# Kernel tuning notes

Measured on AMD Instinct MI355X. Metric: run time of the kernel, lower is better.

Reference implementation:

```python
import math
import jax, jax.numpy as jnp
import numpy as np

NUM_HEADS = 32
HEAD_DIM = 128
POOL = 16
MAX_REL = 8192
RMS_EPS = 1e-6


def _central_mask_features(distances, feature_size, seq_length):
    # center_widths = arange(F) + geomspace(1, seq_length-F+1, F, endpoint=False)
    log_end = math.log(float(seq_length - feature_size + 1))
    log_step = log_end / feature_size
    exponents = jnp.arange(feature_size, dtype=jnp.float32) * log_step
    center_widths = jnp.arange(feature_size, dtype=jnp.float32) + jnp.exp(exponents)
    return (center_widths > distances[..., None]).astype(jnp.float32)


def _shift(x, query_length, key_length):
    # x: [..., n_rows, n_diags] with n_diags = 2*n_rows
    batch_shape = x.shape[:-2]
    n_rows, n_diags = x.shape[-2], x.shape[-1]
    x = x.reshape(*batch_shape, n_diags, n_rows)
    x = x[..., 1:, :]
    x = x.reshape(*batch_shape, n_rows, n_diags - 1)
    return x[..., :key_length]


def setup_inputs() -> dict:
    key = jax.random.key(0)
    ks = jax.random.split(key, 12)
    B, S, D = 1, 8192, 1536
    HD = NUM_HEADS * HEAD_DIM  # 4096
    s = 0.02
    return {
        "x": jax.random.normal(ks[0], (B, S, D), jnp.float32),
        "w_rms": jnp.ones((D,), jnp.float32),
        "W_q": jax.random.normal(ks[1], (D, HD), jnp.float32) * s,
        "W_k": jax.random.normal(ks[2], (D, HD), jnp.float32) * s,
        "W_pos": jax.random.normal(ks[3], (2 * NUM_HEADS, HD), jnp.float32) * s,
        "b_pos": jnp.zeros((HD,), jnp.float32),
        "q_r_bias": jax.random.normal(ks[4], (1, 1, NUM_HEADS, HEAD_DIM), jnp.float32) * s,
        "k_r_bias": jax.random.normal(ks[5], (1, 1, NUM_HEADS, HEAD_DIM), jnp.float32) * s,
        "W_yq": jax.random.normal(ks[6], (D, HEAD_DIM), jnp.float32) * s,
        "W_yk": jax.random.normal(ks[7], (D, HEAD_DIM), jnp.float32) * s,
        "W_pair": jax.random.normal(ks[8], (NUM_HEADS, HEAD_DIM), jnp.float32) * s,
        "b_pair": jnp.zeros((HEAD_DIM,), jnp.float32),
    }


def reference(x, w_rms, W_q, W_k, W_pos, b_pos, q_r_bias, k_r_bias, W_yq, W_yk, W_pair, b_pair):
    B, S, D = x.shape
    Sp = S // POOL
    # mean-pool along sequence (kernel=stride=16)
    x_pooled = x.reshape(B, Sp, POOL, D).mean(axis=2)
    # RMSNorm
    x_norm = x_pooled * jax.lax.rsqrt(jnp.mean(x_pooled * x_pooled, axis=-1, keepdims=True) + RMS_EPS) * w_rms

    q = (x_norm @ W_q).reshape(B, Sp, NUM_HEADS, HEAD_DIM)
    k = (x_norm @ W_k).reshape(B, Sp, NUM_HEADS, HEAD_DIM)

    # relative-position features
    range_vec = jnp.arange(-Sp, Sp, dtype=jnp.float32)
    pos_feat = _central_mask_features(jnp.abs(range_vec), NUM_HEADS, MAX_REL // POOL)  # [2Sp, H]
    sign = jnp.sign(range_vec)[:, None]
    pos_feat = jnp.concatenate([pos_feat, sign * pos_feat], axis=-1)  # [2Sp, 2H]
    pos_enc = (pos_feat @ W_pos + b_pos).reshape(2 * Sp, NUM_HEADS, HEAD_DIM)

    term_q = jnp.einsum('bqhc,phc->bhqp', q + q_r_bias, pos_enc)
    term_k = jnp.einsum('bkhc,phc->bhkp', k + k_r_bias, pos_enc)
    rel_q_a = _shift(term_q, Sp, Sp)  # [B,H,Q,K]
    rel_k_a = _shift(term_k, Sp, Sp)
    rel_q_a = jnp.transpose(rel_q_a, (0, 2, 3, 1))  # [B,Q,K,H]
    rel_k_a = jnp.transpose(rel_k_a, (0, 3, 2, 1))  # [B,P,K,H]

    a = jnp.einsum('bqhc,bkhc->bqkh', q, k)
    a = a + 0.5 * (rel_q_a + rel_k_a)

    x_gelu = jax.nn.gelu(x_norm, approximate=False)
    y_q = x_gelu @ W_yq  # [B,Sp,HEAD_DIM]
    y_k = x_gelu @ W_yk

    pair_act = a @ W_pair + b_pair + y_q[:, :, None, :] + y_k[:, None, :, :]
    return pair_act
```

## Files before the change

### kernel.cpp

```cpp
#include <hip/hip_runtime.h>
#include <hip/hip_bf16.h>
#include <math.h>
#include <stdint.h>

#define NHEADS 32
#define HDIM 128
#define POOLW 16
#define DMODEL 1536
#define SPOOL 512
#define HDTOT 4096
#define PEROWS 1024
#define NPAIR (SPOOL * SPOOL)
#define TCOLS 80

typedef __hip_bfloat16 bf16;
typedef short short8 __attribute__((ext_vector_type(8)));
typedef float f32x4 __attribute__((ext_vector_type(4)));

__device__ __forceinline__ float b2f(const bf16 v) { return __bfloat162float(v); }
__device__ __forceinline__ bf16 f2b(float v) { return __float2bfloat16(v); }
__device__ __forceinline__ short f2bs(float v) {
  bf16 b = __float2bfloat16(v);
  return *reinterpret_cast<short*>(&b);
}

__device__ __forceinline__ void gload_lds16(const void* g, void* l) {
  const __attribute__((address_space(1))) uint32_t* gp =
      (const __attribute__((address_space(1))) uint32_t*)(uintptr_t)g;
  __attribute__((address_space(3))) uint32_t* lp =
      (__attribute__((address_space(3))) uint32_t*)(uintptr_t)l;
  __builtin_amdgcn_global_load_lds(gp, lp, 16, 0, 0);
}

__global__ __launch_bounds__(256) void pool_suffix(
    const float* __restrict__ x, const float* __restrict__ w_rms,
    const float* __restrict__ W_pos,
    bf16* __restrict__ xn, bf16* __restrict__ xg,
    float* __restrict__ SW0, float* __restrict__ SW1) {
  if (blockIdx.x >= SPOOL) {
    int j = (blockIdx.x - SPOOL) * 256 + threadIdx.x;
    float s0 = 0.f, s1 = 0.f;
    SW0[32 * HDTOT + j] = 0.f;
    SW1[32 * HDTOT + j] = 0.f;
    for (int f = 31; f >= 0; --f) {
      s0 += W_pos[f * HDTOT + j];
      s1 += W_pos[(NHEADS + f) * HDTOT + j];
      SW0[f * HDTOT + j] = s0;
      SW1[f * HDTOT + j] = s1;
    }
    return;
  }
  int sp = blockIdx.x;
  int tid = threadIdx.x;
  __shared__ float buf[DMODEL];
  __shared__ float red[256];
  const float* xrow = x + (size_t)sp * POOLW * DMODEL;
  float ss = 0.f;
  for (int d = tid; d < DMODEL; d += 256) {
    float s = 0.f;
#pragma unroll
    for (int p = 0; p < POOLW; ++p) s += xrow[p * DMODEL + d];
    s *= (1.0f / POOLW);
    buf[d] = s;
    ss += s * s;
  }
  red[tid] = ss;
  __syncthreads();
  for (int off = 128; off > 0; off >>= 1) {
    if (tid < off) red[tid] += red[tid + off];
    __syncthreads();
  }
  float rms = rsqrtf(red[0] / DMODEL + 1e-6f);
  for (int d = tid; d < DMODEL; d += 256) {
    float v = buf[d] * rms * w_rms[d];
    xn[(size_t)sp * DMODEL + d] = f2b(v);
    xg[(size_t)sp * DMODEL + d] = f2b(0.5f * v * (1.0f + erff(v * 0.70710678118654752f)));
  }
}

__global__ __launch_bounds__(256) void prep_kernel(
    const float* __restrict__ SW0, const float* __restrict__ SW1,
    const float* __restrict__ b_pos, const float* __restrict__ qrb,
    const float* __restrict__ krb, const float* __restrict__ W_pair,
    bf16* __restrict__ SWb, float* __restrict__ RB, short* __restrict__ fm_tab,
    bf16* __restrict__ WpT) {
  int b = blockIdx.x, t = threadIdx.x;
  if (b < 32) {
    int h = b;
    bf16* dst = SWb + (size_t)h * 128 * 128;
    for (int rr = 0; rr < 128; rr += 2) {
      int g = rr + (t >> 7);
      int c = t & 127;
      float v;
      if (g < 33) v = SW0[(size_t)g * HDTOT + h * 128 + c];
      else if (g < 66) v = SW1[(size_t)(g - 33) * HDTOT + h * 128 + c];
      else if (g == 66) v = b_pos[h * 128 + c];
      else v = 0.f;
      dst[(size_t)g * 128 + c] = f2b(v);
    }
  } else if (b < 96) {
    int idx = b - 32;
    int s = idx >> 5, h = idx & 31;
    const float* rb = (s ? krb : qrb) + h * 128;
    if (t < 128) {
      int g = t;
      float acc = 0.f;
      if (g < 33) { for (int c = 0; c < 128; ++c) acc += rb[c] * SW0[(size_t)g * HDTOT + h * 128 + c]; }
      else if (g < 66) { for (int c = 0; c < 128; ++c) acc += rb[c] * SW1[(size_t)(g - 33) * HDTOT + h * 128 + c]; }
      else if (g == 66) { for (int c = 0; c < 128; ++c) acc += rb[c] * b_pos[h * 128 + c]; }
      RB[(size_t)idx * 128 + g] = acc;
    }
  } else if (b == 96) {
    for (int p = t; p < 1024; p += 256) {
      float dist = fabsf((float)(p - 512));
      double ls = log(481.0) / 32.0;
      int fmv = 0;
      for (int f = 0; f < 32; ++f) {
        float cw = (float)f + expf((float)f * (float)ls);
        if (cw <= dist) fmv = f + 1;
      }
      fm_tab[p] = (short)fmv;
    }
  } else {
    for (int idx = t; idx < NHEADS * HDIM; idx += 256) {
      int c = idx >> 5, h = idx & 31;
      WpT[(size_t)c * 32 + h] = f2b(W_pair[h * HDIM + c]);
    }
  }
}

__global__ __launch_bounds__(256) void gemm_proj32(
    const bf16* __restrict__ xn, const bf16* __restrict__ xg,
    const float* __restrict__ W_q, const float* __restrict__ W_k,
    const float* __restrict__ W_yq, const float* __restrict__ W_yk,
    bf16* __restrict__ QKp, float* __restrict__ yqk) {
  __shared__ short Asub[256][32];
  __shared__ short Bsub[32][40];
  const int t = threadIdx.x;
  const int lane = t & 63, w = t >> 6;
  const int quad = lane >> 4, mr = lane & 15;
  const int bx = blockIdx.x;
  const int m0 = blockIdx.y * 256;
  const int wm = w * 64;

  const bf16* A;
  const float* Wb;
  int ncol, ldw;
  if (bx < 256) {
    A = xn;
    int n0 = bx * 32;
    if (n0 < 4096) { Wb = W_q; ncol = n0; } else { Wb = W_k; ncol = n0 - 4096; }
    ldw = 4096;
  } else {
    A = xg;
    int n0 = (bx - 256) * 32;
    if (n0 < 128) { Wb = W_yq; ncol = n0; } else { Wb = W_yk; ncol = n0 - 128; }
    ldw = 128;
  }

  int a_r[4], a_c[4];
#pragma unroll
  for (int j = 0; j < 4; ++j) {
    int c = t + j * 256;
    int r = c >> 2, pc = c & 3;
    a_r[j] = r;
    a_c[j] = (pc ^ (r & 3)) * 8;
  }
  const int kr = t >> 3, nq = t & 7;

  f32x4 acc[4][2];
#pragma unroll
  for (int mi = 0; mi < 4; ++mi)
#pragma unroll
    for (int ni = 0; ni < 2; ++ni) acc[mi][ni] = (f32x4){0.f, 0.f, 0.f, 0.f};

  for (int k0 = 0; k0 < DMODEL; k0 += 32) {
#pragma unroll
    for (int j = 0; j < 4; ++j)
      gload_lds16(A + (size_t)(m0 + a_r[j]) * DMODEL + k0 + a_c[j],
                  (char*)&Asub[0][0] + (size_t)(t + j * 256) * 16);
    {
      f32x4 wv = *(const f32x4*)&Wb[(size_t)(k0 + kr) * ldw + ncol + nq * 4];
      Bsub[nq * 4 + 0][kr] = f2bs(wv[0]);
      Bsub[nq * 4 + 1][kr] = f2bs(wv[1]);
      Bsub[nq * 4 + 2][kr] = f2bs(wv[2]);
      Bsub[nq * 4 + 3][kr] = f2bs(wv[3]);
    }
    __syncthreads();
    short8 af[4];
#pragma unroll
    for (int mi = 0; mi < 4; ++mi) {
      int r = wm + mi * 16 + mr;
      af[mi] = *(const short8*)&Asub[r][(quad ^ (r & 3)) * 8];
    }
    short8 bfr[2];
#pragma unroll
    for (int ni = 0; ni < 2; ++ni) {
      int rb = ni * 16 + mr;
      bfr[ni] = *(const short8*)&Bsub[rb][quad * 8];
    }
#pragma unroll
    for (int mi = 0; mi < 4; ++mi)
#pragma unroll
      for (int ni = 0; ni < 2; ++ni)
        acc[mi][ni] = __builtin_amdgcn_mfma_f32_16x16x32_bf16(af[mi], bfr[ni], acc[mi][ni], 0, 0, 0);
    __syncthreads();
  }

#pragma unroll
  for (int mi = 0; mi < 4; ++mi) {
#pragma unroll
    for (int ni = 0; ni < 2; ++ni) {
#pragma unroll
      for (int r = 0; r < 4; ++r) {
        int gm = m0 + wm + mi * 16 + quad * 4 + r;
        int gnl = ni * 16 + mr;
        float v = acc[mi][ni][r];
        if (bx < 256) {
          QKp[(size_t)gm * 8192 + bx * 32 + gnl] = f2b(v);
        } else {
          yqk[(size_t)gm * 256 + (bx - 256) * 32 + gnl] = v;
        }
      }
    }
  }
}

__global__ __launch_bounds__(256) void gemm_table(
    const bf16* __restrict__ QKp, const bf16* __restrict__ SWb,
    const float* __restrict__ RB, float* __restrict__ Tg) {
  __shared__ short Asub[128][32];
  __shared__ short Bsub[64][32];
  const int t = threadIdx.x;
  const int lane = t & 63;
  const int w = t >> 6;
  const int z = blockIdx.z;
  const int m0 = blockIdx.y * 128, n0 = blockIdx.x * 64;
  const int wm = (w >> 1) * 64, wn = (w & 1) * 32;
  const bf16* Ag = QKp + (size_t)(z >> 5) * 4096 + (size_t)(z & 31) * 128;
  const bf16* Bg = SWb + (size_t)(z & 31) * 128 * 128;

  const int ar0 = t >> 2;
  const int as0 = t & 3;
  const int ao0 = as0 ^ (ar0 & 3);
  char* AsubB = (char*)&Asub[0][0];
  char* BsubB = (char*)&Bsub[0][0];
  char* ldsA0 = AsubB + w * 1024;
  char* ldsA1 = AsubB + 4096 + w * 1024;
  char* ldsB0 = BsubB + w * 1024;

  const int quad = lane >> 4, mr = lane & 15;
  f32x4 acc[4][2];
#pragma unroll
  for (int mi = 0; mi < 4; ++mi)
#pragma unroll
    for (int ni = 0; ni < 2; ++ni) acc[mi][ni] = (f32x4){0.f, 0.f, 0.f, 0.f};

  for (int k0 = 0; k0 < 128; k0 += 32) {
    gload_lds16(Ag + (size_t)(m0 + ar0) * 8192 + k0 + ao0 * 8, ldsA0);
    gload_lds16(Ag + (size_t)(m0 + 64 + ar0) * 8192 + k0 + ao0 * 8, ldsA1);
    gload_lds16(Bg + (size_t)(n0 + ar0) * 128 + k0 + ao0 * 8, ldsB0);
    __syncthreads();
    short8 af[4];
#pragma unroll
    for (int mi = 0; mi < 4; ++mi) {
      int r = wm + mi * 16 + mr;
      af[mi] = *(const short8*)&Asub[r][(quad ^ (r & 3)) * 8];
    }
    short8 bfr[2];
#pragma unroll
    for (int ni = 0; ni < 2; ++ni) {
      int r = wn + ni * 16 + mr;
      bfr[ni] = *(const short8*)&Bsub[r][(quad ^ (r & 3)) * 8];
    }
#pragma unroll
    for (int mi = 0; mi < 4; ++mi)
#pragma unroll
      for (int ni = 0; ni < 2; ++ni)
        acc[mi][ni] = __builtin_amdgcn_mfma_f32_16x16x32_bf16(af[mi], bfr[ni], acc[mi][ni], 0, 0, 0);
    __syncthreads();
  }

  float* Cz = Tg + (size_t)z * 512 * TCOLS;
  const float* ex = RB + (size_t)z * 128;
#pragma unroll
  for (int mi = 0; mi < 4; ++mi) {
#pragma unroll
    for (int ni = 0; ni < 2; ++ni) {
#pragma unroll
      for (int r = 0; r < 4; ++r) {
        int gm = m0 + wm + mi * 16 + quad * 4 + r;
        int gn = n0 + wn + ni * 16 + mr;
        if (gn < TCOLS) Cz[(size_t)gm * TCOLS + gn] = acc[mi][ni][r] + ex[gn];
      }
    }
  }
}

#define MEGA_LDS 161920
__global__ __launch_bounds__(512) void mega_kernel(
    const bf16* __restrict__ QKp, const float* __restrict__ Tg,
    const short* __restrict__ fm_tab, const bf16* __restrict__ WpT,
    const float* __restrict__ b_pair, const float* __restrict__ yqk,
    float* __restrict__ out) {
  extern __shared__ char sm[];
  float* Ssc = (float*)(sm + 73728);
  short* fmL = (short*)(sm + 77952);
  short* Pl = (short*)(sm + 80000);

  const int t = threadIdx.x;
  const int lane = t & 63, w = t >> 6;
  const int quad = lane >> 4, mr = lane & 15;
  const int q0 = (blockIdx.x >> 4) * 32;
  const int k0 = (blockIdx.x & 15) * 32;

  const int ttc = (t >= 256) ? (t - 256) : 0;
  int qk_r[2], qk_c[2];
#pragma unroll
  for (int j = 0; j < 2; ++j) {
    int c = ttc + j * 256;
    int ks = c >> 7, cc = c & 127;
    int r = cc >> 2, pc = cc & 3;
    qk_r[j] = r;
    qk_c[j] = ks * 32 + ((pc ^ (r & 3)) * 8);
  }
  const int t_n = (t >= 256 && ttc < 128) ? 3 : 2;
  int t_row[3], t_off[3];
#pragma unroll
  for (int j = 0; j < 3; ++j) {
    int c = ttc + j * 256;
    t_row[j] = c / 20;
    t_off[j] = (c - t_row[j] * 20) * 4;
  }

#define STAGE_ALL(hh)                                                                  \
  {                                                                                    \
    int bsel = (hh) & 1;                                                               \
    char* qdst = sm + bsel * 8192;                                                     \
    char* kdst = sm + 16384 + bsel * 8192;                                             \
    char* tqdst = sm + 32768 + bsel * 10240;                                           \
    char* tkdst = sm + 53248 + bsel * 10240;                                           \
    const float* sq_ = Tg + (size_t)(hh)*512 * TCOLS;                                  \
    const float* sk_ = Tg + (size_t)(32 + (hh)) * 512 * TCOLS;                         \
    _Pragma("unroll")                                                                  \
    for (int j = 0; j < 2; ++j) {                                                      \
      int c = ttc + j * 256;                                                           \
      gload_lds16(QKp + (size_t)(q0 + qk_r[j]) * 8192 + (hh)*128 + qk_c[j],            \
                  qdst + (size_t)c * 16);                                              \
      gload_lds16(QKp + (size_t)(k0 + qk_r[j]) * 8192 + 4096 + (hh)*128 + qk_c[j],     \
                  kdst + (size_t)c * 16);                                              \
    }                                                                                  \
    for (int j = 0; j < t_n; ++j) {                                                    \
      int c = ttc + j * 256;                                                           \
      gload_lds16(sq_ + (size_t)(q0 + t_row[j]) * TCOLS + t_off[j],                    \
                  tqdst + (size_t)c * 16);                                             \
      gload_lds16(sk_ + (size_t)(k0 + t_row[j]) * TCOLS + t_off[j],                    \
                  tkdst + (size_t)c * 16);                                             \
    }                                                                                  \
  }

  if (t < 128) gload_lds16(fm_tab + t * 8, (char*)fmL + t * 16);
  if (t >= 256) STAGE_ALL(0);
  __syncthreads();

  int tqa[2], tqb[2], tqc[2], tka[2], tkb[2], tkc[2], ssco[2], plo[2];
  float sgn[2];
#pragma unroll
  for (int j = 0; j < 2; ++j) {
    int m = j * 512 + t;
    int qL = m >> 5, kL = m & 31;
    int pq = 512 + (k0 + kL) - (q0 + qL);
    int gq = fmL[pq], gk = fmL[1024 - pq];
    sgn[j] = (pq > 512) ? 1.f : ((pq < 512) ? -1.f : 0.f);
    tqa[j] = qL * TCOLS + gq;
    tqb[j] = qL * TCOLS + 33 + gq;
    tqc[j] = qL * TCOLS + 66;
    tka[j] = kL * TCOLS + gk;
    tkb[j] = kL * TCOLS + 33 + gk;
    tkc[j] = kL * TCOLS + 66;
    ssco[j] = qL * 33 + kL;
    plo[j] = m * 40;
  }

  for (int h = 0; h < 32; ++h) {
    if (w < 4) {
      const short* Qb = (const short*)(sm + (h & 1) * 8192);
      const short* Kb = (const short*)(sm + 16384 + (h & 1) * 8192);
      const int smi = w >> 1, sni = w & 1;
      const int ra = smi * 16 + mr, rb = sni * 16 + mr;
      f32x4 accS = (f32x4){0.f, 0.f, 0.f, 0.f};
#pragma unroll
      for (int ks = 0; ks < 4; ++ks) {
        short8 af = *(const short8*)&Qb[ks * 1024 + ra * 32 + ((quad ^ (ra & 3)) * 8)];
        short8 bfv = *(const short8*)&Kb[ks * 1024 + rb * 32 + ((quad ^ (rb & 3)) * 8)];
        accS = __builtin_amdgcn_mfma_f32_16x16x32_bf16(af, bfv, accS, 0, 0, 0);
      }
#pragma unroll
      for (int r = 0; r < 4; ++r)
        Ssc[(smi * 16 + quad * 4 + r) * 33 + sni * 16 + mr] = accS[r];
    } else if (h < 31) {
      STAGE_ALL(h + 1);
    }
    __syncthreads();
    {
      const float* tq = (const float*)(sm + 32768 + (h & 1) * 10240);
      const float* tk = (const float*)(sm + 53248 + (h & 1) * 10240);
#pragma unroll
      for (int j = 0; j < 2; ++j) {
        float vq = tq[tqa[j]] + sgn[j] * tq[tqb[j]] + tq[tqc[j]];
        float vk = tk[tka[j]] - sgn[j] * tk[tkb[j]] + tk[tkc[j]];
        float val = Ssc[ssco[j]] + 0.5f * (vq + vk);
        Pl[plo[j] + h] = f2bs(val);
      }
    }
    __syncthreads();
  }

  short8 bfr[8];
  float bp[8];
#pragma unroll
  for (int ni = 0; ni < 8; ++ni) {
    int c = ni * 16 + mr;
    bfr[ni] = *(const short8*)(WpT + (size_t)c * 32 + quad * 8);
    bp[ni] = b_pair[c];
  }
#pragma unroll
  for (int mi = 0; mi < 8; ++mi) {
    int mb = w * 128 + mi * 16;
    short8 af = *(const short8*)&Pl[(mb + mr) * 40 + quad * 8];
    f32x4 acc[8];
#pragma unroll
    for (int ni = 0; ni < 8; ++ni)
      acc[ni] = __builtin_amdgcn_mfma_f32_16x16x32_bf16(
          af, bfr[ni], (f32x4){0.f, 0.f, 0.f, 0.f}, 0, 0, 0);
#pragma unroll
    for (int r = 0; r < 4; ++r) {
      int m = mb + quad * 4 + r;
      int q = q0 + (m >> 5), k = k0 + (m & 31);
      const float* yq = yqk + (size_t)q * 256;
      const float* yk = yqk + (size_t)k * 256 + 128;
      float* orow = out + ((size_t)q * 512 + k) * 128;
#pragma unroll
      for (int ni = 0; ni < 8; ++ni) {
        int c = ni * 16 + mr;
        orow[c] = acc[ni][r] + bp[ni] + yq[c] + yk[c];
      }
    }
  }
}

extern "C" void kernel_launch(void* const* d_in, const int* in_sizes, int n_in,
                              void* d_out, int out_size, void* d_ws, size_t ws_size,
                              hipStream_t stream) {
  const float* x      = (const float*)d_in[0];
  const float* w_rms  = (const float*)d_in[1];
  const float* W_q    = (const float*)d_in[2];
  const float* W_k    = (const float*)d_in[3];
  const float* W_pos  = (const float*)d_in[4];
  const float* b_pos  = (const float*)d_in[5];
  const float* qrb    = (const float*)d_in[6];
  const float* krb    = (const float*)d_in[7];
  const float* W_yq   = (const float*)d_in[8];
  const float* W_yk   = (const float*)d_in[9];
  const float* W_pair = (const float*)d_in[10];
  const float* b_pair = (const float*)d_in[11];
  float* out = (float*)d_out;

  static bool attr_set = false;
  if (!attr_set) {
    (void)hipFuncSetAttribute((const void*)mega_kernel,
                              hipFuncAttributeMaxDynamicSharedMemorySize, MEGA_LDS);
    attr_set = true;
  }

  char* w = (char*)d_ws;
  bf16* xn   = (bf16*)w; w += (size_t)SPOOL * DMODEL * 2;
  bf16* xg   = (bf16*)w; w += (size_t)SPOOL * DMODEL * 2;
  bf16* QKp  = (bf16*)w; w += (size_t)SPOOL * 8192 * 2;
  float* yqk = (float*)w; w += (size_t)SPOOL * 256 * 4;
  bf16* WpT  = (bf16*)w; w += (size_t)HDIM * NHEADS * 2;
  float* SW0 = (float*)w; w += (size_t)33 * HDTOT * 4;
  float* SW1 = (float*)w; w += (size_t)33 * HDTOT * 4;
  bf16* SWb  = (bf16*)w; w += (size_t)NHEADS * 128 * 128 * 2;
  float* RB  = (float*)w; w += (size_t)64 * 128 * 4;
  short* fm_tab = (short*)w; w += 1024 * 2;
  w = (char*)(((uintptr_t)w + 255) & ~(uintptr_t)255);
  float* Tg = (float*)w; w += (size_t)2 * NHEADS * SPOOL * TCOLS * 4;

  pool_suffix<<<SPOOL + HDTOT / 256, 256, 0, stream>>>(x, w_rms, W_pos, xn, xg, SW0, SW1);
  prep_kernel<<<98, 256, 0, stream>>>(SW0, SW1, b_pos, qrb, krb, W_pair,
                                      SWb, RB, fm_tab, WpT);
  gemm_proj32<<<dim3(264, 2), 256, 0, stream>>>(
      xn, xg, W_q, W_k, W_yq, W_yk, QKp, yqk);
  gemm_table<<<dim3(128 / 64, SPOOL / 128, 64), 256, 0, stream>>>(QKp, SWb, RB, Tg);
  mega_kernel<<<256, 512, MEGA_LDS, stream>>>(QKp, Tg, fm_tab, WpT, b_pair, yqk, out);
}
```

Before: 364.3 us.

## Shrink mega_kernel tiles to 32x16 and keep pair activations in registers

The fused pair kernel now uses 32x16 query-key tiles over 512 blocks instead of 32x32 tiles over 256 blocks. The per-head pair activations are built straight into MFMA A-operand registers instead of a large LDS staging buffer, which cuts LDS from about 160KB to about 48KB and should allow more blocks per CU. Table rows are prefetched through registers into a double-buffered LDS area, but Q/K now use a single buffer, so there are more barriers per head. Each 16-row group of lanes (quad) handles one group of 8 heads, so only a quarter of the lanes do the elementwise work in each head step.

```diff
diff --git a/kernel.cpp b/kernel.cpp
--- a/kernel.cpp
+++ b/kernel.cpp
@@ -12,6 +12,7 @@
 #define PEROWS 1024
 #define NPAIR (SPOOL * SPOOL)
 #define TCOLS 80
+#define TLDS 84
 
 typedef __hip_bfloat16 bf16;
 typedef short short8 __attribute__((ext_vector_type(8)));
@@ -297,123 +298,129 @@
   }
 }
 
-#define MEGA_LDS 161920
+#define MEGA_LDS 48768
 __global__ __launch_bounds__(512) void mega_kernel(
     const bf16* __restrict__ QKp, const float* __restrict__ Tg,
     const short* __restrict__ fm_tab, const bf16* __restrict__ WpT,
     const float* __restrict__ b_pair, const float* __restrict__ yqk,
     float* __restrict__ out) {
   extern __shared__ char sm[];
-  float* Ssc = (float*)(sm + 73728);
-  short* fmL = (short*)(sm + 77952);
-  short* Pl = (short*)(sm + 80000);
+  float* Ssc = (float*)(sm + 44544);
+  short* fmL = (short*)(sm + 46720);
 
   const int t = threadIdx.x;
   const int lane = t & 63, w = t >> 6;
   const int quad = lane >> 4, mr = lane & 15;
-  const int q0 = (blockIdx.x >> 4) * 32;
-  const int k0 = (blockIdx.x & 15) * 32;
-
-  const int ttc = (t >= 256) ? (t - 256) : 0;
-  int qk_r[2], qk_c[2];
-#pragma unroll
-  for (int j = 0; j < 2; ++j) {
-    int c = ttc + j * 256;
-    int ks = c >> 7, cc = c & 127;
-    int r = cc >> 2, pc = cc & 3;
-    qk_r[j] = r;
-    qk_c[j] = ks * 32 + ((pc ^ (r & 3)) * 8);
-  }
-  const int t_n = (t >= 256 && ttc < 128) ? 3 : 2;
-  int t_row[3], t_off[3];
-#pragma unroll
-  for (int j = 0; j < 3; ++j) {
-    int c = ttc + j * 256;
-    t_row[j] = c / 20;
-    t_off[j] = (c - t_row[j] * 20) * 4;
-  }
-
-#define STAGE_ALL(hh)                                                                  \
-  {                                                                                    \
-    int bsel = (hh) & 1;                                                               \
-    char* qdst = sm + bsel * 8192;                                                     \
-    char* kdst = sm + 16384 + bsel * 8192;                                             \
-    char* tqdst = sm + 32768 + bsel * 10240;                                           \
-    char* tkdst = sm + 53248 + bsel * 10240;                                           \
-    const float* sq_ = Tg + (size_t)(hh)*512 * TCOLS;                                  \
-    const float* sk_ = Tg + (size_t)(32 + (hh)) * 512 * TCOLS;                         \
-    _Pragma("unroll")                                                                  \
-    for (int j = 0; j < 2; ++j) {                                                      \
-      int c = ttc + j * 256;                                                           \
-      gload_lds16(QKp + (size_t)(q0 + qk_r[j]) * 8192 + (hh)*128 + qk_c[j],            \
-                  qdst + (size_t)c * 16);                                              \
-      gload_lds16(QKp + (size_t)(k0 + qk_r[j]) * 8192 + 4096 + (hh)*128 + qk_c[j],     \
-                  kdst + (size_t)c * 16);                                              \
-    }                                                                                  \
-    for (int j = 0; j < t_n; ++j) {                                                    \
-      int c = ttc + j * 256;                                                           \
-      gload_lds16(sq_ + (size_t)(q0 + t_row[j]) * TCOLS + t_off[j],                    \
-                  tqdst + (size_t)c * 16);                                             \
-      gload_lds16(sk_ + (size_t)(k0 + t_row[j]) * TCOLS + t_off[j],                    \
-                  tkdst + (size_t)c * 16);                                             \
-    }                                                                                  \
-  }
-
-  if (t < 128) gload_lds16(fm_tab + t * 8, (char*)fmL + t * 16);
-  if (t >= 256) STAGE_ALL(0);
+  const int q0 = (blockIdx.x >> 5) * 32;
+  const int k0 = (blockIdx.x & 31) * 16;
+
+  const int qc_r = (t & 127) >> 2;
+  const int qcol = (t >> 7) * 32 + (((t & 3) ^ (qc_r & 3)) * 8);
+  const int kc_r = (t & 63) >> 2;
+  const int kcol = ((t >> 6) & 3) * 32 + (((t & 3) ^ (kc_r & 3)) * 8);
+
+  const int tr1 = t / 20, to1 = (t % 20) * 4;
+  const int ti1 = tr1 * TLDS + to1;
+  const int c2 = 512 + t;
+  const int tr2 = c2 / 20, to2 = (c2 % 20) * 4;
+  const int ti2 = (tr2 < 32) ? tr2 * TLDS + to2 : 2688 + (tr2 - 32) * TLDS + to2;
+  const bool hasB = (t < 448);
+
+  {
+    const float* sq_ = Tg;
+    const float* sk_ = Tg + (size_t)32 * SPOOL * TCOLS;
+    f32x4 pA = *(const f32x4*)(sq_ + (size_t)(q0 + tr1) * TCOLS + to1);
+    f32x4 pB = (f32x4){0.f, 0.f, 0.f, 0.f};
+    if (hasB) {
+      const float* s2 = (tr2 < 32) ? sq_ + (size_t)(q0 + tr2) * TCOLS + to2
+                                   : sk_ + (size_t)(k0 + tr2 - 32) * TCOLS + to2;
+      pB = *(const f32x4*)s2;
+    }
+    gload_lds16(QKp + (size_t)(q0 + qc_r) * 8192 + qcol, sm + t * 16);
+    if (t < 256)
+      gload_lds16(QKp + (size_t)(k0 + kc_r) * 8192 + 4096 + kcol, sm + 8192 + t * 16);
+    if (t < 128) gload_lds16(fm_tab + t * 8, (char*)fmL + t * 16);
+    float* dT = (float*)(sm + 12288);
+    *(f32x4*)&dT[ti1] = pA;
+    if (hasB) *(f32x4*)&dT[ti2] = pB;
+  }
   __syncthreads();
 
-  int tqa[2], tqb[2], tqc[2], tka[2], tkb[2], tkc[2], ssco[2], plo[2];
-  float sgn[2];
-#pragma unroll
-  for (int j = 0; j < 2; ++j) {
-    int m = j * 512 + t;
-    int qL = m >> 5, kL = m & 31;
+  int tqa[4], tqc[4], tka[4], tkc[4], ssco[4];
+  float sgnv[4];
+#pragma unroll
+  for (int mi = 0; mi < 4; ++mi) {
+    int m = w * 64 + mi * 16 + mr;
+    int qL = m >> 4, kL = m & 15;
     int pq = 512 + (k0 + kL) - (q0 + qL);
     int gq = fmL[pq], gk = fmL[1024 - pq];
-    sgn[j] = (pq > 512) ? 1.f : ((pq < 512) ? -1.f : 0.f);
-    tqa[j] = qL * TCOLS + gq;
-    tqb[j] = qL * TCOLS + 33 + gq;
-    tqc[j] = qL * TCOLS + 66;
-    tka[j] = kL * TCOLS + gk;
-    tkb[j] = kL * TCOLS + 33 + gk;
-    tkc[j] = kL * TCOLS + 66;
-    ssco[j] = qL * 33 + kL;
-    plo[j] = m * 40;
-  }
-
-  for (int h = 0; h < 32; ++h) {
-    if (w < 4) {
-      const short* Qb = (const short*)(sm + (h & 1) * 8192);
-      const short* Kb = (const short*)(sm + 16384 + (h & 1) * 8192);
-      const int smi = w >> 1, sni = w & 1;
-      const int ra = smi * 16 + mr, rb = sni * 16 + mr;
-      f32x4 accS = (f32x4){0.f, 0.f, 0.f, 0.f};
-#pragma unroll
-      for (int ks = 0; ks < 4; ++ks) {
-        short8 af = *(const short8*)&Qb[ks * 1024 + ra * 32 + ((quad ^ (ra & 3)) * 8)];
-        short8 bfv = *(const short8*)&Kb[ks * 1024 + rb * 32 + ((quad ^ (rb & 3)) * 8)];
-        accS = __builtin_amdgcn_mfma_f32_16x16x32_bf16(af, bfv, accS, 0, 0, 0);
-      }
-#pragma unroll
-      for (int r = 0; r < 4; ++r)
-        Ssc[(smi * 16 + quad * 4 + r) * 33 + sni * 16 + mr] = accS[r];
-    } else if (h < 31) {
-      STAGE_ALL(h + 1);
-    }
-    __syncthreads();
-    {
-      const float* tq = (const float*)(sm + 32768 + (h & 1) * 10240);
-      const float* tk = (const float*)(sm + 53248 + (h & 1) * 10240);
-#pragma unroll
-      for (int j = 0; j < 2; ++j) {
-        float vq = tq[tqa[j]] + sgn[j] * tq[tqb[j]] + tq[tqc[j]];
-        float vk = tk[tka[j]] - sgn[j] * tk[tkb[j]] + tk[tkc[j]];
-        float val = Ssc[ssco[j]] + 0.5f * (vq + vk);
-        Pl[plo[j] + h] = f2bs(val);
-      }
-    }
-    __syncthreads();
+    sgnv[mi] = (pq > 512) ? 1.f : ((pq < 512) ? -1.f : 0.f);
+    tqa[mi] = qL * TLDS + gq;
+    tqc[mi] = qL * TLDS + 66;
+    tka[mi] = 2688 + kL * TLDS + gk;
+    tkc[mi] = 2688 + kL * TLDS + 66;
+    ssco[mi] = qL * 17 + kL;
+  }
+
+  short8 af[4];
+
+  for (int hg = 0; hg < 4; ++hg) {
+#pragma unroll
+    for (int hj = 0; hj < 8; ++hj) {
+      const int h = hg * 8 + hj;
+      const bool notlast = (h < 31);
+      f32x4 tA = (f32x4){0.f, 0.f, 0.f, 0.f}, tB = (f32x4){0.f, 0.f, 0.f, 0.f};
+      if (notlast) {
+        const float* sq_ = Tg + (size_t)(h + 1) * SPOOL * TCOLS;
+        const float* sk_ = Tg + (size_t)(33 + h) * SPOOL * TCOLS;
+        tA = *(const f32x4*)(sq_ + (size_t)(q0 + tr1) * TCOLS + to1);
+        if (hasB) {
+          const float* s2 = (tr2 < 32) ? sq_ + (size_t)(q0 + tr2) * TCOLS + to2
+                                       : sk_ + (size_t)(k0 + tr2 - 32) * TCOLS + to2;
+          tB = *(const f32x4*)s2;
+        }
+      }
+      if (w < 2) {
+        const short* Qb = (const short*)sm;
+        const short* Kb = (const short*)(sm + 8192);
+        const int ra = w * 16 + mr;
+        f32x4 accS = (f32x4){0.f, 0.f, 0.f, 0.f};
+#pragma unroll
+        for (int ks = 0; ks < 4; ++ks) {
+          short8 a = *(const short8*)&Qb[ks * 1024 + ra * 32 + ((quad ^ (ra & 3)) * 8)];
+          short8 b = *(const short8*)&Kb[ks * 512 + mr * 32 + ((quad ^ (mr & 3)) * 8)];
+          accS = __builtin_amdgcn_mfma_f32_16x16x32_bf16(a, b, accS, 0, 0, 0);
+        }
+#pragma unroll
+        for (int r = 0; r < 4; ++r)
+          Ssc[(w * 16 + quad * 4 + r) * 17 + mr] = accS[r];
+      }
+      asm volatile("s_waitcnt lgkmcnt(0)" ::: "memory");
+      __builtin_amdgcn_s_barrier();
+      __builtin_amdgcn_sched_barrier(0);
+      if (quad == hg) {
+        const float* Tl = (const float*)(sm + 12288 + (hj & 1) * 16128);
+#pragma unroll
+        for (int mi = 0; mi < 4; ++mi) {
+          float s = sgnv[mi];
+          float vq = Tl[tqa[mi]] + s * Tl[tqa[mi] + 33] + Tl[tqc[mi]];
+          float vk = Tl[tka[mi]] - s * Tl[tka[mi] + 33] + Tl[tkc[mi]];
+          float val = Ssc[ssco[mi]] + 0.5f * (vq + vk);
+          af[mi][hj] = f2bs(val);
+        }
+      }
+      if (notlast) {
+        float* dT = (float*)(sm + 12288 + ((hj + 1) & 1) * 16128);
+        *(f32x4*)&dT[ti1] = tA;
+        if (hasB) *(f32x4*)&dT[ti2] = tB;
+        gload_lds16(QKp + (size_t)(q0 + qc_r) * 8192 + (h + 1) * 128 + qcol,
+                    sm + t * 16);
+        if (t < 256)
+          gload_lds16(QKp + (size_t)(k0 + kc_r) * 8192 + 4096 + (h + 1) * 128 + kcol,
+                      sm + 8192 + t * 16);
+      }
+      __syncthreads();
+    }
   }
 
   short8 bfr[8];
@@ -425,18 +432,16 @@
     bp[ni] = b_pair[c];
   }
 #pragma unroll
-  for (int mi = 0; mi < 8; ++mi) {
-    int mb = w * 128 + mi * 16;
-    short8 af = *(const short8*)&Pl[(mb + mr) * 40 + quad * 8];
+  for (int mi = 0; mi < 4; ++mi) {
     f32x4 acc[8];
 #pragma unroll
     for (int ni = 0; ni < 8; ++ni)
       acc[ni] = __builtin_amdgcn_mfma_f32_16x16x32_bf16(
-          af, bfr[ni], (f32x4){0.f, 0.f, 0.f, 0.f}, 0, 0, 0);
+          af[mi], bfr[ni], (f32x4){0.f, 0.f, 0.f, 0.f}, 0, 0, 0);
 #pragma unroll
     for (int r = 0; r < 4; ++r) {
-      int m = mb + quad * 4 + r;
-      int q = q0 + (m >> 5), k = k0 + (m & 31);
+      int m = w * 64 + mi * 16 + quad * 4 + r;
+      int q = q0 + (m >> 4), k = k0 + (m & 15);
       const float* yq = yqk + (size_t)q * 256;
       const float* yk = yqk + (size_t)k * 256 + 128;
       float* orow = out + ((size_t)q * 512 + k) * 128;
@@ -493,5 +498,5 @@
   gemm_proj32<<<dim3(264, 2), 256, 0, stream>>>(
       xn, xg, W_q, W_k, W_yq, W_yk, QKp, yqk);
   gemm_table<<<dim3(128 / 64, SPOOL / 128, 64), 256, 0, stream>>>(QKp, SWb, RB, Tg);
-  mega_kernel<<<256, 512, MEGA_LDS, stream>>>(QKp, Tg, fm_tab, WpT, b_pair, yqk, out);
-}
+  mega_kernel<<<512, 512, MEGA_LDS, stream>>>(QKp, Tg, fm_tab, WpT, b_pair, yqk, out);
+}
```

Result: faster. 350.5 us (-3.8%).
